# Kernel optimization log

Measured on AMD Instinct MI355X. Metric: run time of the kernel, lower is better.

Reference implementation:

```python
import jax, jax.numpy as jnp
import numpy as np

B, N, D, H = 128, 32768, 768, 16
DH = D // H          # per-head hidden_size = memory_dim // num_heads = 48
BETA = 0.25          # scaling (inverse temperature)
STEPS = 5            # update_steps_max
TOPK = 4


def _ln(x, g, b):
    # torch nn.LayerNorm over last dim (biased variance, eps=1e-5), affine
    m = jnp.mean(x, axis=-1, keepdims=True)
    v = jnp.var(x, axis=-1, keepdims=True)
    return (x - m) * jax.lax.rsqrt(v + 1e-5) * g + b


def _l2norm(x):
    # F.normalize(x, dim=-1): x / max(||x||, 1e-12)
    n = jnp.linalg.norm(x, axis=-1, keepdims=True)
    return x / jnp.maximum(n, 1e-12)


def setup_inputs() -> dict:
    key = jax.random.key(0)
    ks = jax.random.split(key, 8)
    s = 0.05  # weight init scale to keep activations sane
    return {
        "query_embedding": jax.random.normal(ks[0], (B, D), jnp.float32),
        "memory_bank": jax.random.normal(ks[1], (N, D), jnp.float32),
        "ln_k_g": jnp.ones((D,), jnp.float32), "ln_k_b": jnp.zeros((D,), jnp.float32),
        "ln_q_g": jnp.ones((D,), jnp.float32), "ln_q_b": jnp.zeros((D,), jnp.float32),
        "ln_v_g": jnp.ones((D,), jnp.float32), "ln_v_b": jnp.zeros((D,), jnp.float32),
        "Wq": jax.random.normal(ks[2], (D, D), jnp.float32) * s, "bq": jnp.zeros((D,), jnp.float32),
        "Wk": jax.random.normal(ks[3], (D, D), jnp.float32) * s, "bk": jnp.zeros((D,), jnp.float32),
        "Wv": jax.random.normal(ks[4], (D, D), jnp.float32) * s, "bv": jnp.zeros((D,), jnp.float32),
        "Wo": jax.random.normal(ks[5], (D, D), jnp.float32) * s, "bo": jnp.zeros((D,), jnp.float32),
        "W1": jax.random.normal(ks[6], (D, D), jnp.float32) * s, "b1": jnp.zeros((D,), jnp.float32),
        "W2": jax.random.normal(ks[7], (D, D), jnp.float32) * s, "b2": jnp.zeros((D,), jnp.float32),
    }


def reference(query_embedding, memory_bank, ln_k_g, ln_k_b, ln_q_g, ln_q_b,
              ln_v_g, ln_v_b, Wq, bq, Wk, bk, Wv, bv, Wo, bo, W1, b1, W2, b2):
    # Affine LayerNorms on stored pattern, state pattern, pattern projection.
    # memory_bank is shared across the batch, so normalize/project it ONCE
    # instead of materializing the (B, N, D) expand from the torch code.
    stored = _ln(memory_bank, ln_k_g, ln_k_b)        # (N, D)
    state = _ln(query_embedding, ln_q_g, ln_q_b)     # (B, D) -- state pattern, seq len 1
    projp = _ln(memory_bank, ln_v_g, ln_v_b)         # (N, D)

    k = (stored @ Wk.T + bk).reshape(N, H, DH)       # (N, H, dh)
    v = (projp @ Wv.T + bv).reshape(N, H, DH)        # (N, H, dh)
    q = (state @ Wq.T + bq).reshape(B, H, DH)        # (B, H, dh)

    # Hopfield convergence: xi <- softmax(beta * xi K^T) K, repeated STEPS times
    def step(xi, _):
        attn = jax.nn.softmax(BETA * jnp.einsum('bhd,nhd->bhn', xi, k), axis=-1)
        return jnp.einsum('bhn,nhd->bhd', attn, k), None

    xi, _ = jax.lax.scan(step, q, None, length=STEPS)

    # Final readout against the (separately normalized) pattern projection V
    attn = jax.nn.softmax(BETA * jnp.einsum('bhd,nhd->bhn', xi, k), axis=-1)  # (B, H, N)
    converged = jnp.einsum('bhn,nhd->bhd', attn, v).reshape(B, D) @ Wo.T + bo  # (B, D)

    # Retrieval head: residual + MLP + cosine-sim logits + top-k
    combined = query_embedding + converged
    rq = jax.nn.relu(combined @ W1.T + b1) @ W2.T + b2
    logits = (_l2norm(rq) @ _l2norm(memory_bank).T) * 20.0   # (B, N)
    top_indices = jax.lax.top_k(logits, TOPK)[1]              # (B, TOPK)
    return top_indices, logits
```

## Files before the change

kernel.cpp:

```cpp
#include <hip/hip_runtime.h>
#include <math.h>

#define NTOT 32768
#define DMODEL 768
#define BSZ 128
#define NHEAD 16
#define DH 48
#define BETA 0.25f

typedef _Float16 f16;
typedef f16 f16x8 __attribute__((ext_vector_type(8)));
typedef f16 f16x4 __attribute__((ext_vector_type(4)));
typedef float f32x4 __attribute__((ext_vector_type(4)));

__global__ __launch_bounds__(256)
void row_stats(const float* __restrict__ X, int M, float* __restrict__ mean,
               float* __restrict__ rstd, float* __restrict__ l2inv) {
  const int row = blockIdx.x * 4 + (threadIdx.x >> 6);
  const int lane = threadIdx.x & 63;
  if (row >= M) return;
  const float* x = X + (size_t)row * DMODEL;
  float s = 0.f, s2 = 0.f;
  for (int i = lane; i < DMODEL; i += 64) {
    float v = x[i];
    s += v; s2 += v * v;
  }
#pragma unroll
  for (int off = 32; off; off >>= 1) {
    s  += __shfl_xor(s, off);
    s2 += __shfl_xor(s2, off);
  }
  if (lane == 0) {
    float mu = s * (1.f / DMODEL);
    float var = s2 * (1.f / DMODEL) - mu * mu;
    mean[row] = mu;
    rstd[row] = rsqrtf(var + 1e-5f);
    if (l2inv) l2inv[row] = 1.f / fmaxf(sqrtf(s2), 1e-12f);
  }
}

__global__ __launch_bounds__(256)
void norm_split_mb(const float* __restrict__ mb, const float* __restrict__ mean,
                   const float* __restrict__ rstd, f16* __restrict__ nh_hi,
                   f16* __restrict__ nh_lo) {
  const int row = blockIdx.x * 4 + (threadIdx.x >> 6);
  const int lane = threadIdx.x & 63;
  const float mu = mean[row];
  const float rs = rstd[row];
  const float* x = mb + (size_t)row * DMODEL;
  f16* oh = nh_hi + (size_t)row * DMODEL;
  f16* ol = nh_lo + (size_t)row * DMODEL;
  for (int d = lane * 4; d < DMODEL; d += 256) {
    const float4 v = *(const float4*)(x + d);
    const float s[4] = {(v.x - mu) * rs, (v.y - mu) * rs,
                        (v.z - mu) * rs, (v.w - mu) * rs};
    f16x4 h4, l4;
#pragma unroll
    for (int j = 0; j < 4; j++) {
      const f16 h = (f16)s[j];
      h4[j] = h;
      l4[j] = (f16)(s[j] - (float)h);
    }
    *(f16x4*)(oh + d) = h4;
    *(f16x4*)(ol + d) = l4;
  }
}

__global__ __launch_bounds__(256)
void prep_w(const float* __restrict__ Wk, const float* __restrict__ bk,
            const float* __restrict__ gk, const float* __restrict__ blnk,
            const float* __restrict__ Wv, const float* __restrict__ bv,
            const float* __restrict__ gv, const float* __restrict__ blnv,
            f16* __restrict__ Wc_hi, f16* __restrict__ Wc_lo,
            float* __restrict__ biasc) {
  const int o = blockIdx.x * 4 + (threadIdx.x >> 6);
  const int lane = threadIdx.x & 63;
  const bool isK = o < DMODEL;
  const float* W = isK ? (Wk + (size_t)o * DMODEL)
                       : (Wv + (size_t)(o - DMODEL) * DMODEL);
  const float* g   = isK ? gk : gv;
  const float* bln = isK ? blnk : blnv;
  float bacc = 0.f;
  for (int d = lane * 4; d < DMODEL; d += 256) {
    const float4 wv = *(const float4*)(W + d);
    const float4 g4 = *(const float4*)(g + d);
    const float4 b4 = *(const float4*)(bln + d);
    bacc += wv.x * b4.x + wv.y * b4.y + wv.z * b4.z + wv.w * b4.w;
    const float sv[4] = {wv.x * g4.x * 16.f, wv.y * g4.y * 16.f,
                         wv.z * g4.z * 16.f, wv.w * g4.w * 16.f};
    f16x4 h4, l4;
#pragma unroll
    for (int j = 0; j < 4; j++) {
      const f16 h = (f16)sv[j];
      h4[j] = h;
      l4[j] = (f16)(sv[j] - (float)h);
    }
    *(f16x4*)(Wc_hi + (size_t)o * DMODEL + d) = h4;
    *(f16x4*)(Wc_lo + (size_t)o * DMODEL + d) = l4;
  }
#pragma unroll
  for (int off = 32; off; off >>= 1) bacc += __shfl_xor(bacc, off);
  if (lane == 0) biasc[o] = (isK ? bk[o] : bv[o - DMODEL]) + bacc;
}

__global__ __launch_bounds__(256)
void proj_dual_mfma(const f16* __restrict__ nh_hi, const f16* __restrict__ nh_lo,
                    const f16* __restrict__ Wc_hi, const f16* __restrict__ Wc_lo,
                    const float* __restrict__ biasc,
                    f16* __restrict__ k_hi, f16* __restrict__ k_lo,
                    f16* __restrict__ v_hi, f16* __restrict__ v_lo) {
  __shared__ __align__(16) f16 As[128][64];
  __shared__ __align__(16) f16 Bs[128][64];
  const int t = threadIdx.x;
  const int n0 = blockIdx.x * 128;
  const int m0 = blockIdx.y * 128;
  const int w = t >> 6, lane = t & 63;
  const int l15 = lane & 15, lq = lane >> 4;
  const int wm = w >> 1, wn = w & 1;
  const int sc = (lane & 7) ^ (lane >> 3);
  const int srow = lane >> 3;

  f32x4 acc[4][4];
#pragma unroll
  for (int a = 0; a < 4; a++)
#pragma unroll
    for (int b = 0; b < 4; b++)
#pragma unroll
      for (int r = 0; r < 4; r++) acc[a][b][r] = 0.f;

  for (int k0 = 0; k0 < DMODEL; k0 += 32) {
    __syncthreads();
#pragma unroll
    for (int i = 0; i < 4; i++) {
      const int rb = (w * 4 + i) * 8;
      const f16* asrc = ((sc < 4) ? nh_hi : nh_lo) +
          (size_t)(m0 + rb + srow) * DMODEL + k0 + (sc & 3) * 8;
      __builtin_amdgcn_global_load_lds(
          (__attribute__((address_space(1))) void*)asrc,
          (__attribute__((address_space(3))) void*)&As[rb][0], 16, 0, 0);
      const f16* bsrc = ((sc < 4) ? Wc_hi : Wc_lo) +
          (size_t)(n0 + rb + srow) * DMODEL + k0 + (sc & 3) * 8;
      __builtin_amdgcn_global_load_lds(
          (__attribute__((address_space(1))) void*)bsrc,
          (__attribute__((address_space(3))) void*)&Bs[rb][0], 16, 0, 0);
    }
    __syncthreads();

    f16x8 nhh[4], nhl[4];
#pragma unroll
    for (int fm = 0; fm < 4; fm++) {
      const int row = wm * 64 + fm * 16 + l15;
      const int e = row & 7;
      nhh[fm] = *(const f16x8*)&As[row][(lq ^ e) * 8];
      nhl[fm] = *(const f16x8*)&As[row][((lq + 4) ^ e) * 8];
    }
    f16x8 wh[4], wl[4];
#pragma unroll
    for (int fo = 0; fo < 4; fo++) {
      const int row = wn * 64 + fo * 16 + l15;
      const int e = row & 7;
      wh[fo] = *(const f16x8*)&Bs[row][(lq ^ e) * 8];
      wl[fo] = *(const f16x8*)&Bs[row][((lq + 4) ^ e) * 8];
    }
#pragma unroll
    for (int fo = 0; fo < 4; fo++)
#pragma unroll
      for (int fm = 0; fm < 4; fm++) {
        f32x4 a = acc[fo][fm];
        a = __builtin_amdgcn_mfma_f32_16x16x32_f16(wh[fo], nhh[fm], a, 0, 0, 0);
        a = __builtin_amdgcn_mfma_f32_16x16x32_f16(wh[fo], nhl[fm], a, 0, 0, 0);
        a = __builtin_amdgcn_mfma_f32_16x16x32_f16(wl[fo], nhh[fm], a, 0, 0, 0);
        acc[fo][fm] = a;
      }
  }
  const int oc = n0 + wn * 64;
  const bool isK = oc < DMODEL;
  f16* oh = isK ? k_hi : v_hi;
  f16* ol = isK ? k_lo : v_lo;
  const int obase = (isK ? oc : oc - DMODEL) + lq * 4;
#pragma unroll
  for (int fo = 0; fo < 4; fo++) {
    const float4 bb = *(const float4*)(biasc + oc + fo * 16 + lq * 4);
    const float bbv[4] = {bb.x, bb.y, bb.z, bb.w};
    const int o = obase + fo * 16;
#pragma unroll
    for (int fm = 0; fm < 4; fm++) {
      const size_t moff = (size_t)(m0 + wm * 64 + fm * 16 + l15) * DMODEL + o;
      f16x4 h4, l4;
#pragma unroll
      for (int r = 0; r < 4; r++) {
        const float v = acc[fo][fm][r] * 0.0625f + bbv[r];
        const f16 h = (f16)v;
        h4[r] = h;
        l4[r] = (f16)(v - (float)h);
      }
      *(f16x4*)(oh + moff) = h4;
      *(f16x4*)(ol + moff) = l4;
    }
  }
}

__global__ __launch_bounds__(256)
void ln_gemm_f32(const float* __restrict__ A, const float* __restrict__ mean,
                 const float* __restrict__ rstd, const float* __restrict__ g,
                 const float* __restrict__ bln, const float* __restrict__ W,
                 const float* __restrict__ bias, float* __restrict__ out) {
  __shared__ float As[16][68];
  __shared__ float Ws[16][68];
  const int t = threadIdx.x;
  const int m0 = blockIdx.y << 6, n0 = blockIdx.x << 6;
  const int tm = t >> 4, tn = t & 15;
  const int lr = t >> 2;
  const int lk = (t & 3) << 2;
  const float muL = mean[m0 + lr];
  const float rsL = rstd[m0 + lr];
  float acc[4][4] = {};
  for (int k0 = 0; k0 < DMODEL; k0 += 16) {
    float4 a4 = *(const float4*)(A + (size_t)(m0 + lr) * DMODEL + k0 + lk);
    float4 g4 = *(const float4*)(g + k0 + lk);
    float4 b4 = *(const float4*)(bln + k0 + lk);
    As[lk + 0][lr] = (a4.x - muL) * rsL * g4.x + b4.x;
    As[lk + 1][lr] = (a4.y - muL) * rsL * g4.y + b4.y;
    As[lk + 2][lr] = (a4.z - muL) * rsL * g4.z + b4.z;
    As[lk + 3][lr] = (a4.w - muL) * rsL * g4.w + b4.w;
    float4 w4 = *(const float4*)(W + (size_t)(n0 + lr) * DMODEL + k0 + lk);
    Ws[lk + 0][lr] = w4.x;
    Ws[lk + 1][lr] = w4.y;
    Ws[lk + 2][lr] = w4.z;
    Ws[lk + 3][lr] = w4.w;
    __syncthreads();
#pragma unroll
    for (int kk = 0; kk < 16; kk++) {
      const float4 av = *(const float4*)(&As[kk][tm * 4]);
      const float4 bv = *(const float4*)(&Ws[kk][tn * 4]);
      const float a[4] = {av.x, av.y, av.z, av.w};
      const float b[4] = {bv.x, bv.y, bv.z, bv.w};
#pragma unroll
      for (int i = 0; i < 4; i++)
#pragma unroll
        for (int j = 0; j < 4; j++) acc[i][j] += a[i] * b[j];
    }
    __syncthreads();
  }
  const float4 bia = *(const float4*)(bias + n0 + tn * 4);
  const float bb[4] = {bia.x, bia.y, bia.z, bia.w};
#pragma unroll
  for (int i = 0; i < 4; i++) {
    const int m = m0 + tm * 4 + i;
    float4 o4;
    o4.x = acc[i][0] + bb[0];
    o4.y = acc[i][1] + bb[1];
    o4.z = acc[i][2] + bb[2];
    o4.w = acc[i][3] + bb[3];
    *(float4*)(out + (size_t)m * DMODEL + n0 + tn * 4) = o4;
  }
}

__global__ __launch_bounds__(256)
void gemm_bias(const float* __restrict__ A, const float* __restrict__ W,
               const float* __restrict__ bias, const float* __restrict__ add,
               float* __restrict__ out, int relu) {
  __shared__ float As[16][68];
  __shared__ float Ws[16][68];
  const int t = threadIdx.x;
  const int m0 = blockIdx.y << 6, n0 = blockIdx.x << 6;
  const int tm = t >> 4, tn = t & 15;
  const int lr = t >> 2;
  const int lk = (t & 3) << 2;
  float acc[4][4] = {};
  for (int k0 = 0; k0 < DMODEL; k0 += 16) {
    float4 a4 = *(const float4*)(A + (size_t)(m0 + lr) * DMODEL + k0 + lk);
    As[lk + 0][lr] = a4.x;
    As[lk + 1][lr] = a4.y;
    As[lk + 2][lr] = a4.z;
    As[lk + 3][lr] = a4.w;
    float4 w4 = *(const float4*)(W + (size_t)(n0 + lr) * DMODEL + k0 + lk);
    Ws[lk + 0][lr] = w4.x;
    Ws[lk + 1][lr] = w4.y;
    Ws[lk + 2][lr] = w4.z;
    Ws[lk + 3][lr] = w4.w;
    __syncthreads();
#pragma unroll
    for (int kk = 0; kk < 16; kk++) {
      const float4 av = *(const float4*)(&As[kk][tm * 4]);
      const float4 bv = *(const float4*)(&Ws[kk][tn * 4]);
      const float a[4] = {av.x, av.y, av.z, av.w};
      const float b[4] = {bv.x, bv.y, bv.z, bv.w};
#pragma unroll
      for (int i = 0; i < 4; i++)
#pragma unroll
        for (int j = 0; j < 4; j++) acc[i][j] += a[i] * b[j];
    }
    __syncthreads();
  }
  const float4 bia = *(const float4*)(bias + n0 + tn * 4);
  const float bb[4] = {bia.x, bia.y, bia.z, bia.w};
#pragma unroll
  for (int i = 0; i < 4; i++) {
    const int m = m0 + tm * 4 + i;
    float v[4];
#pragma unroll
    for (int j = 0; j < 4; j++) v[j] = acc[i][j] + bb[j];
    if (add) {
      const float4 a4 = *(const float4*)(add + (size_t)m * DMODEL + n0 + tn * 4);
      v[0] += a4.x; v[1] += a4.y; v[2] += a4.z; v[3] += a4.w;
    }
    if (relu) {
#pragma unroll
      for (int j = 0; j < 4; j++) v[j] = fmaxf(v[j], 0.f);
    }
    float4 o4 = {v[0], v[1], v[2], v[3]};
    *(float4*)(out + (size_t)m * DMODEL + n0 + tn * 4) = o4;
  }
}

__global__ __launch_bounds__(256)
void logits_gemm(const float* __restrict__ A, const float* __restrict__ Bm,
                 const float* __restrict__ ainv, const float* __restrict__ binv,
                 float* __restrict__ out) {
  __shared__ float As[16][68];
  __shared__ float Ws[16][68];
  const int t = threadIdx.x;
  const int m0 = blockIdx.y << 6, n0 = blockIdx.x << 6;
  const int tm = t >> 4, tn = t & 15;
  const int lr = t >> 2;
  const int lk = (t & 3) << 2;
  float acc[4][4] = {};
  for (int k0 = 0; k0 < DMODEL; k0 += 16) {
    float4 a4 = *(const float4*)(A + (size_t)(m0 + lr) * DMODEL + k0 + lk);
    As[lk + 0][lr] = a4.x;
    As[lk + 1][lr] = a4.y;
    As[lk + 2][lr] = a4.z;
    As[lk + 3][lr] = a4.w;
    float4 w4 = *(const float4*)(Bm + (size_t)(n0 + lr) * DMODEL + k0 + lk);
    Ws[lk + 0][lr] = w4.x;
    Ws[lk + 1][lr] = w4.y;
    Ws[lk + 2][lr] = w4.z;
    Ws[lk + 3][lr] = w4.w;
    __syncthreads();
#pragma unroll
    for (int kk = 0; kk < 16; kk++) {
      const float4 av = *(const float4*)(&As[kk][tm * 4]);
      const float4 bv = *(const float4*)(&Ws[kk][tn * 4]);
      const float a[4] = {av.x, av.y, av.z, av.w};
      const float b[4] = {bv.x, bv.y, bv.z, bv.w};
#pragma unroll
      for (int i = 0; i < 4; i++)
#pragma unroll
        for (int j = 0; j < 4; j++) acc[i][j] += a[i] * b[j];
    }
    __syncthreads();
  }
  const float4 bi4 = *(const float4*)(binv + n0 + tn * 4);
  const float bi[4] = {bi4.x, bi4.y, bi4.z, bi4.w};
#pragma unroll
  for (int i = 0; i < 4; i++) {
    const int m = m0 + tm * 4 + i;
    const float sa = 20.f * ainv[m];
    float4 o4;
    o4.x = acc[i][0] * sa * bi[0];
    o4.y = acc[i][1] * sa * bi[1];
    o4.z = acc[i][2] * sa * bi[2];
    o4.w = acc[i][3] * sa * bi[3];
    *(float4*)(out + (size_t)m * NTOT + n0 + tn * 4) = o4;
  }
}

__global__ __launch_bounds__(256)
void split_xi_k(const float* __restrict__ xi, f16* __restrict__ hi,
                f16* __restrict__ lo) {
  const int i = blockIdx.x * 256 + threadIdx.x;
  float4 v = ((const float4*)xi)[i];
  float s[4] = {v.x * BETA, v.y * BETA, v.z * BETA, v.w * BETA};
  f16x4 h4, l4;
#pragma unroll
  for (int j = 0; j < 4; j++) {
    f16 h = (f16)s[j];
    h4[j] = h;
    l4[j] = (f16)(s[j] - (float)h);
  }
  ((f16x4*)hi)[i] = h4;
  ((f16x4*)lo)[i] = l4;
}

#define FCHUNK 64
#define FROWS (NTOT / FCHUNK)

__global__ __launch_bounds__(256)
void flash_round(const f16* __restrict__ k_hi, const f16* __restrict__ k_lo,
                 const f16* __restrict__ val_hi, const f16* __restrict__ val_lo,
                 const f16* __restrict__ xi_hi, const f16* __restrict__ xi_lo,
                 float* __restrict__ part_ml, float* __restrict__ part_o) {
  const int h = blockIdx.y, chunk = blockIdx.x;
  const int tid = threadIdx.x, w = tid >> 6, lane = tid & 63;
  const int l15 = lane & 15, lq = lane >> 4;
  const int b0 = w * 32;

  __shared__ __align__(16) f16 krow[2][32][56];
  __shared__ __align__(16) f16 vT[2][48][40];
  __shared__ __align__(16) f16 pHi[4][32][40];
  __shared__ __align__(16) f16 pLo[4][32][40];

  const f16x8 zf = {};
  f16x8 xqh[2][2], xql[2][2];
#pragma unroll
  for (int bt = 0; bt < 2; bt++) {
    const size_t xoff = (size_t)(b0 + bt * 16 + l15) * DMODEL + h * DH;
    xqh[bt][0] = *(const f16x8*)(xi_hi + xoff + lq * 8);
    xql[bt][0] = *(const f16x8*)(xi_lo + xoff + lq * 8);
    const size_t xo1 = xoff + 32 + (lq & 1) * 8;
    f16x8 th = *(const f16x8*)(xi_hi + xo1);
    f16x8 tl = *(const f16x8*)(xi_lo + xo1);
    xqh[bt][1] = (lq < 2) ? th : zf;
    xql[bt][1] = (lq < 2) ? tl : zf;
  }

  float m[2] = {-1e30f, -1e30f}, lsum[2] = {0.f, 0.f};
  f32x4 O[3][2];
#pragma unroll
  for (int mt = 0; mt < 3; mt++)
#pragma unroll
    for (int bt = 0; bt < 2; bt++)
#pragma unroll
      for (int j = 0; j < 4; j++) O[mt][bt][j] = 0.f;

  const int nbase = chunk * FROWS;
  for (int it = 0; it < FROWS / 32; it++) {
    const int gn0 = nbase + it * 32;
    __syncthreads();
    for (int j = tid; j < 384; j += 256) {
      const int tsel = j / 192;
      const int q = j - tsel * 192;
      const int r = q / 6;
      const int d0 = (q - r * 6) * 8;
      const size_t goff = (size_t)(gn0 + r) * DMODEL + h * DH + d0;
      const f16* kp = (tsel ? k_lo : k_hi) + goff;
      const f16* vp = (tsel ? val_lo : val_hi) + goff;
      f16x8 kv = *(const f16x8*)kp;
      f16x8 vv = *(const f16x8*)vp;
      *(f16x8*)&krow[tsel][r][d0] = kv;
#pragma unroll
      for (int jj = 0; jj < 8; jj++) vT[tsel][d0 + jj][r] = vv[jj];
    }
    __syncthreads();

    f16x8 akh[2][2], akl[2][2];
#pragma unroll
    for (int nt = 0; nt < 2; nt++) {
      const int row = nt * 16 + l15;
      akh[nt][0] = *(const f16x8*)&krow[0][row][lq * 8];
      akl[nt][0] = *(const f16x8*)&krow[1][row][lq * 8];
      f16x8 t0 = *(const f16x8*)&krow[0][row][32 + (lq & 1) * 8];
      f16x8 t1 = *(const f16x8*)&krow[1][row][32 + (lq & 1) * 8];
      akh[nt][1] = (lq < 2) ? t0 : zf;
      akl[nt][1] = (lq < 2) ? t1 : zf;
    }
    f32x4 S[2][2];
#pragma unroll
    for (int nt = 0; nt < 2; nt++)
#pragma unroll
      for (int bt = 0; bt < 2; bt++) {
        f32x4 s = {};
        s = __builtin_amdgcn_mfma_f32_16x16x32_f16(akh[nt][0], xqh[bt][0], s, 0, 0, 0);
        s = __builtin_amdgcn_mfma_f32_16x16x32_f16(akh[nt][1], xqh[bt][1], s, 0, 0, 0);
        s = __builtin_amdgcn_mfma_f32_16x16x32_f16(akh[nt][0], xql[bt][0], s, 0, 0, 0);
        s = __builtin_amdgcn_mfma_f32_16x16x32_f16(akh[nt][1], xql[bt][1], s, 0, 0, 0);
        s = __builtin_amdgcn_mfma_f32_16x16x32_f16(akl[nt][0], xqh[bt][0], s, 0, 0, 0);
        s = __builtin_amdgcn_mfma_f32_16x16x32_f16(akl[nt][1], xqh[bt][1], s, 0, 0, 0);
        S[nt][bt] = s;
      }
    float sc[2];
#pragma unroll
    for (int bt = 0; bt < 2; bt++) {
      float mx = S[0][bt][0];
#pragma unroll
      for (int r = 1; r < 4; r++) mx = fmaxf(mx, S[0][bt][r]);
#pragma unroll
      for (int r = 0; r < 4; r++) mx = fmaxf(mx, S[1][bt][r]);
      mx = fmaxf(mx, __shfl_xor(mx, 16));
      mx = fmaxf(mx, __shfl_xor(mx, 32));
      const float mnew = fmaxf(m[bt], mx);
      sc[bt] = __expf(m[bt] - mnew);
      float ps = 0.f;
#pragma unroll
      for (int nt = 0; nt < 2; nt++) {
        f16x4 ph, pl;
#pragma unroll
        for (int r = 0; r < 4; r++) {
          const float p = __expf(S[nt][bt][r] - mnew);
          ps += p;
          const f16 hh = (f16)p;
          ph[r] = hh;
          pl[r] = (f16)(p - (float)hh);
        }
        *(f16x4*)&pHi[w][bt * 16 + l15][nt * 16 + lq * 4] = ph;
        *(f16x4*)&pLo[w][bt * 16 + l15][nt * 16 + lq * 4] = pl;
      }
      ps += __shfl_xor(ps, 16);
      ps += __shfl_xor(ps, 32);
      lsum[bt] = lsum[bt] * sc[bt] + ps;
      m[bt] = mnew;
    }
    __asm__ volatile("s_waitcnt lgkmcnt(0)" ::: "memory");
    f16x8 avh[3], avl[3];
#pragma unroll
    for (int mt = 0; mt < 3; mt++) {
      avh[mt] = *(const f16x8*)&vT[0][mt * 16 + l15][lq * 8];
      avl[mt] = *(const f16x8*)&vT[1][mt * 16 + l15][lq * 8];
    }
    f16x8 pbh[2], pbl[2];
#pragma unroll
    for (int bt = 0; bt < 2; bt++) {
      pbh[bt] = *(const f16x8*)&pHi[w][bt * 16 + l15][lq * 8];
      pbl[bt] = *(const f16x8*)&pLo[w][bt * 16 + l15][lq * 8];
    }
#pragma unroll
    for (int mt = 0; mt < 3; mt++)
#pragma unroll
      for (int bt = 0; bt < 2; bt++) {
#pragma unroll
        for (int j = 0; j < 4; j++) O[mt][bt][j] *= sc[bt];
        f32x4 o = O[mt][bt];
        o = __builtin_amdgcn_mfma_f32_16x16x32_f16(avh[mt], pbh[bt], o, 0, 0, 0);
        o = __builtin_amdgcn_mfma_f32_16x16x32_f16(avh[mt], pbl[bt], o, 0, 0, 0);
        o = __builtin_amdgcn_mfma_f32_16x16x32_f16(avl[mt], pbh[bt], o, 0, 0, 0);
        O[mt][bt] = o;
      }
  }
  const int pc = h * FCHUNK + chunk;
  if (lq == 0) {
#pragma unroll
    for (int bt = 0; bt < 2; bt++) {
      float* pm = part_ml + ((size_t)pc * BSZ + b0 + bt * 16 + l15) * 2;
      pm[0] = m[bt];
      pm[1] = lsum[bt];
    }
  }
#pragma unroll
  for (int mt = 0; mt < 3; mt++)
#pragma unroll
    for (int bt = 0; bt < 2; bt++) {
      float* po = part_o + ((size_t)pc * BSZ + b0 + bt * 16 + l15) * 48 +
                  mt * 16 + lq * 4;
      *(f32x4*)po = O[mt][bt];
    }
}

__global__ __launch_bounds__(64)
void hopfield_combine(const float* __restrict__ part_ml,
                      const float* __restrict__ part_o, float* __restrict__ dst) {
  const int bh = blockIdx.x;
  const int h = bh >> 7, b = bh & 127;
  const int c = threadIdx.x;
  __shared__ float w[64];
  const float* pm = part_ml + ((size_t)(h * 64 + c) * BSZ + b) * 2;
  const float mp = pm[0];
  const float lp = pm[1];
  float M = mp;
#pragma unroll
  for (int off = 32; off; off >>= 1) M = fmaxf(M, __shfl_xor(M, off));
  const float wp = __expf(mp - M);
  w[c] = wp;
  float L = lp * wp;
#pragma unroll
  for (int off = 32; off; off >>= 1) L += __shfl_xor(L, off);
  __syncthreads();
  if (c < DH) {
    float o = 0.f;
    for (int p = 0; p < 64; p++)
      o += part_o[((size_t)(h * 64 + p) * BSZ + b) * 48 + c] * w[p];
    dst[(size_t)b * DMODEL + h * DH + c] = o / L;
  }
}

__global__ __launch_bounds__(256)
void topk_kernel(const float* __restrict__ logits, float* __restrict__ outIdx) {
  const int b = blockIdx.x;
  const int t = threadIdx.x;
  const float* row = logits + (size_t)b * NTOT;
  float v[4] = {-1e30f, -1e30f, -1e30f, -1e30f};
  int id[4] = {0x7fffffff, 0x7fffffff, 0x7fffffff, 0x7fffffff};
  for (int n = t; n < NTOT; n += 256) {
    const float x = row[n];
    if (x > v[3]) {
      v[3] = x; id[3] = n;
#pragma unroll
      for (int s = 3; s > 0; s--) {
        const bool sw = (v[s] > v[s - 1]) || (v[s] == v[s - 1] && id[s] < id[s - 1]);
        if (sw) {
          float tv = v[s]; v[s] = v[s - 1]; v[s - 1] = tv;
          int ti = id[s]; id[s] = id[s - 1]; id[s - 1] = ti;
        }
      }
    }
  }
  __shared__ float sv[256][4];
  __shared__ int si[256][4];
#pragma unroll
  for (int j = 0; j < 4; j++) { sv[t][j] = v[j]; si[t][j] = id[j]; }
  for (int str = 128; str >= 1; str >>= 1) {
    __syncthreads();
    if (t < str) {
      float a[4], c[4];
      int ai[4], ci[4];
#pragma unroll
      for (int j = 0; j < 4; j++) {
        a[j] = sv[t][j]; ai[j] = si[t][j];
        c[j] = sv[t + str][j]; ci[j] = si[t + str][j];
      }
      float rv[4]; int ri[4];
      int p = 0, q = 0;
#pragma unroll
      for (int oo = 0; oo < 4; oo++) {
        const bool ta = (a[p] > c[q]) || (a[p] == c[q] && ai[p] < ci[q]);
        if (ta) { rv[oo] = a[p]; ri[oo] = ai[p]; p++; }
        else    { rv[oo] = c[q]; ri[oo] = ci[q]; q++; }
      }
#pragma unroll
      for (int j = 0; j < 4; j++) { sv[t][j] = rv[j]; si[t][j] = ri[j]; }
    }
  }
  if (t == 0) {
#pragma unroll
    for (int j = 0; j < 4; j++) outIdx[b * 4 + j] = (float)si[0][j];
  }
}

extern "C" void kernel_launch(void* const* d_in, const int* in_sizes, int n_in,
                              void* d_out, int out_size, void* d_ws, size_t ws_size,
                              hipStream_t stream) {
  const float* qe    = (const float*)d_in[0];
  const float* mb    = (const float*)d_in[1];
  const float* ln_kg = (const float*)d_in[2];
  const float* ln_kb = (const float*)d_in[3];
  const float* ln_qg = (const float*)d_in[4];
  const float* ln_qb = (const float*)d_in[5];
  const float* ln_vg = (const float*)d_in[6];
  const float* ln_vb = (const float*)d_in[7];
  const float* Wq = (const float*)d_in[8];
  const float* bq = (const float*)d_in[9];
  const float* Wk = (const float*)d_in[10];
  const float* bk = (const float*)d_in[11];
  const float* Wv = (const float*)d_in[12];
  const float* bv = (const float*)d_in[13];
  const float* Wo = (const float*)d_in[14];
  const float* bo = (const float*)d_in[15];
  const float* W1 = (const float*)d_in[16];
  const float* b1 = (const float*)d_in[17];
  const float* W2 = (const float*)d_in[18];
  const float* b2 = (const float*)d_in[19];

  float* out = (float*)d_out;
  float* logits = out + BSZ * 4;

  float* ws = (float*)d_ws;
  size_t off = 0;
  auto alloc = [&](size_t n) { float* p = ws + off; off += n; return p; };
  const size_t ND2 = (size_t)NTOT * DMODEL / 2;
  float* mb_mean = alloc(NTOT);
  float* mb_rstd = alloc(NTOT);
  float* mb_l2i  = alloc(NTOT);
  float* q_mean  = alloc(128);
  float* q_rstd  = alloc(128);
  float* rq_inv  = alloc(128);
  float* pad_    = alloc(384);
  f16* k_hi = (f16*)alloc(ND2);
  f16* k_lo = (f16*)alloc(ND2);
  f16* v_hi = (f16*)alloc(ND2);
  f16* v_lo = (f16*)alloc(ND2);
  f16* nh_hi = (f16*)alloc(ND2);
  f16* nh_lo = (f16*)alloc(ND2);
  float* part_ml = alloc((size_t)NHEAD * FCHUNK * BSZ * 2);
  float* part_o  = alloc((size_t)NHEAD * FCHUNK * BSZ * 48);
  float* xi   = alloc((size_t)BSZ * DMODEL);
  float* conv = alloc((size_t)BSZ * DMODEL);
  float* comb = alloc((size_t)BSZ * DMODEL);
  float* h1   = alloc((size_t)BSZ * DMODEL);
  f16* xi_hi = (f16*)alloc((size_t)BSZ * DMODEL / 2);
  f16* xi_lo = (f16*)alloc((size_t)BSZ * DMODEL / 2);
  f16* Wc_hi = (f16*)alloc((size_t)2 * DMODEL * DMODEL / 2);
  f16* Wc_lo = (f16*)alloc((size_t)2 * DMODEL * DMODEL / 2);
  float* biasc = alloc(2 * DMODEL);
  (void)ws_size; (void)in_sizes; (void)n_in; (void)out_size; (void)pad_;

  row_stats<<<NTOT / 4, 256, 0, stream>>>(mb, NTOT, mb_mean, mb_rstd, mb_l2i);
  row_stats<<<BSZ / 4, 256, 0, stream>>>(qe, BSZ, q_mean, q_rstd, nullptr);
  norm_split_mb<<<NTOT / 4, 256, 0, stream>>>(mb, mb_mean, mb_rstd, nh_hi, nh_lo);
  prep_w<<<2 * DMODEL / 4, 256, 0, stream>>>(Wk, bk, ln_kg, ln_kb,
                                             Wv, bv, ln_vg, ln_vb,
                                             Wc_hi, Wc_lo, biasc);

  proj_dual_mfma<<<dim3(2 * DMODEL / 128, NTOT / 128), 256, 0, stream>>>(
      nh_hi, nh_lo, Wc_hi, Wc_lo, biasc, k_hi, k_lo, v_hi, v_lo);
  ln_gemm_f32<<<dim3(DMODEL / 64, BSZ / 64), 256, 0, stream>>>(
      qe, q_mean, q_rstd, ln_qg, ln_qb, Wq, bq, xi);

  for (int r = 0; r < 6; r++) {
    const f16* valHi = (r == 5) ? v_hi : k_hi;
    const f16* valLo = (r == 5) ? v_lo : k_lo;
    float* dst = (r == 5) ? conv : xi;
    split_xi_k<<<96, 256, 0, stream>>>(xi, xi_hi, xi_lo);
    flash_round<<<dim3(FCHUNK, NHEAD), 256, 0, stream>>>(
        k_hi, k_lo, valHi, valLo, xi_hi, xi_lo, part_ml, part_o);
    hopfield_combine<<<BSZ * NHEAD, 64, 0, stream>>>(part_ml, part_o, dst);
  }

  gemm_bias<<<dim3(DMODEL / 64, BSZ / 64), 256, 0, stream>>>(conv, Wo, bo, qe, comb, 0);
  gemm_bias<<<dim3(DMODEL / 64, BSZ / 64), 256, 0, stream>>>(comb, W1, b1, nullptr, h1, 1);
  float* rq = conv;
  gemm_bias<<<dim3(DMODEL / 64, BSZ / 64), 256, 0, stream>>>(h1, W2, b2, nullptr, rq, 0);

  row_stats<<<BSZ / 4, 256, 0, stream>>>(rq, BSZ, q_mean, q_rstd, rq_inv);
  logits_gemm<<<dim3(NTOT / 64, BSZ / 64), 256, 0, stream>>>(rq, mb, rq_inv, mb_l2i, logits);

  topk_kernel<<<BSZ, 256, 0, stream>>>(logits, out);
}
```

Measured before the change: 1.489 ms.

## Compute cosine logits with split-fp16 MFMA on layer-normed bank, fuse mb stats

Replaces the fp32 SIMT logits GEMM with a split-precision (hi/lo fp16) MFMA GEMM. It reuses the already-normalised memory bank halves and recovers raw-bank dot products algebraically as x = n*std + mu, with per-row constants c1 and c2. It also fuses the memory-bank row statistics into the normalise-and-split kernel, removing one full pass over the 100MB bank. The algebraic reconstruction risks precision loss from cancellation between the std and mean terms, which could change top-k ordering.

```diff
diff --git a/kernel.cpp b/kernel.cpp
--- a/kernel.cpp
+++ b/kernel.cpp
@@ -40,29 +40,87 @@
 }
 
 __global__ __launch_bounds__(256)
-void norm_split_mb(const float* __restrict__ mb, const float* __restrict__ mean,
-                   const float* __restrict__ rstd, f16* __restrict__ nh_hi,
-                   f16* __restrict__ nh_lo) {
+void stats_norm_mb(const float* __restrict__ mb, f16* __restrict__ nh_hi,
+                   f16* __restrict__ nh_lo, float* __restrict__ c1,
+                   float* __restrict__ c2) {
   const int row = blockIdx.x * 4 + (threadIdx.x >> 6);
   const int lane = threadIdx.x & 63;
-  const float mu = mean[row];
-  const float rs = rstd[row];
   const float* x = mb + (size_t)row * DMODEL;
+  float v[12];
+  float s = 0.f, s2 = 0.f;
+#pragma unroll
+  for (int j = 0; j < 3; j++) {
+    const float4 v4 = *(const float4*)(x + lane * 4 + j * 256);
+    v[j * 4 + 0] = v4.x; v[j * 4 + 1] = v4.y;
+    v[j * 4 + 2] = v4.z; v[j * 4 + 3] = v4.w;
+    s += v4.x + v4.y + v4.z + v4.w;
+    s2 += v4.x * v4.x + v4.y * v4.y + v4.z * v4.z + v4.w * v4.w;
+  }
+#pragma unroll
+  for (int off = 32; off; off >>= 1) {
+    s  += __shfl_xor(s, off);
+    s2 += __shfl_xor(s2, off);
+  }
+  const float mu = s * (1.f / DMODEL);
+  const float var = s2 * (1.f / DMODEL) - mu * mu;
+  const float istd = sqrtf(var + 1e-5f);
+  const float rs = 1.f / istd;
   f16* oh = nh_hi + (size_t)row * DMODEL;
   f16* ol = nh_lo + (size_t)row * DMODEL;
-  for (int d = lane * 4; d < DMODEL; d += 256) {
-    const float4 v = *(const float4*)(x + d);
-    const float s[4] = {(v.x - mu) * rs, (v.y - mu) * rs,
-                        (v.z - mu) * rs, (v.w - mu) * rs};
+#pragma unroll
+  for (int j = 0; j < 3; j++) {
     f16x4 h4, l4;
 #pragma unroll
-    for (int j = 0; j < 4; j++) {
-      const f16 h = (f16)s[j];
-      h4[j] = h;
-      l4[j] = (f16)(s[j] - (float)h);
+    for (int q = 0; q < 4; q++) {
+      const float sv = (v[j * 4 + q] - mu) * rs;
+      const f16 h = (f16)sv;
+      h4[q] = h;
+      l4[q] = (f16)(sv - (float)h);
+    }
+    *(f16x4*)(oh + lane * 4 + j * 256) = h4;
+    *(f16x4*)(ol + lane * 4 + j * 256) = l4;
+  }
+  if (lane == 0) {
+    const float l2i = 1.f / fmaxf(sqrtf(s2), 1e-12f);
+    c1[row] = 20.f * l2i * istd;
+    c2[row] = 20.f * l2i * mu;
+  }
+}
+
+__global__ __launch_bounds__(256)
+void rq_prep(const float* __restrict__ rq, f16* __restrict__ hi,
+             f16* __restrict__ lo, float* __restrict__ ainv,
+             float* __restrict__ rqsum) {
+  const int row = blockIdx.x * 4 + (threadIdx.x >> 6);
+  const int lane = threadIdx.x & 63;
+  const float* x = rq + (size_t)row * DMODEL;
+  f16* oh = hi + (size_t)row * DMODEL;
+  f16* ol = lo + (size_t)row * DMODEL;
+  float s = 0.f, s2 = 0.f;
+#pragma unroll
+  for (int j = 0; j < 3; j++) {
+    const int d = lane * 4 + j * 256;
+    const float4 v4 = *(const float4*)(x + d);
+    const float vv[4] = {v4.x, v4.y, v4.z, v4.w};
+    f16x4 h4, l4;
+#pragma unroll
+    for (int q = 0; q < 4; q++) {
+      s += vv[q]; s2 += vv[q] * vv[q];
+      const f16 h = (f16)vv[q];
+      h4[q] = h;
+      l4[q] = (f16)(vv[q] - (float)h);
     }
     *(f16x4*)(oh + d) = h4;
     *(f16x4*)(ol + d) = l4;
+  }
+#pragma unroll
+  for (int off = 32; off; off >>= 1) {
+    s  += __shfl_xor(s, off);
+    s2 += __shfl_xor(s2, off);
+  }
+  if (lane == 0) {
+    rqsum[row] = s;
+    ainv[row] = 1.f / fmaxf(sqrtf(s2), 1e-12f);
   }
 }
 
@@ -196,6 +254,98 @@
       }
       *(f16x4*)(oh + moff) = h4;
       *(f16x4*)(ol + moff) = l4;
+    }
+  }
+}
+
+__global__ __launch_bounds__(256)
+void logits_mfma(const f16* __restrict__ nh_hi, const f16* __restrict__ nh_lo,
+                 const f16* __restrict__ rq_hi, const f16* __restrict__ rq_lo,
+                 const float* __restrict__ c1, const float* __restrict__ c2,
+                 const float* __restrict__ ainv, const float* __restrict__ rqsum,
+                 float* __restrict__ out) {
+  __shared__ __align__(16) f16 As[128][64];
+  __shared__ __align__(16) f16 Bs[128][64];
+  const int t = threadIdx.x;
+  const int n0 = blockIdx.x * 128;
+  const int w = t >> 6, lane = t & 63;
+  const int l15 = lane & 15, lq = lane >> 4;
+  const int wm = w >> 1, wn = w & 1;
+  const int sc = (lane & 7) ^ (lane >> 3);
+  const int srow = lane >> 3;
+
+  f32x4 acc[4][4];
+#pragma unroll
+  for (int a = 0; a < 4; a++)
+#pragma unroll
+    for (int b = 0; b < 4; b++)
+#pragma unroll
+      for (int r = 0; r < 4; r++) acc[a][b][r] = 0.f;
+
+  for (int k0 = 0; k0 < DMODEL; k0 += 32) {
+    __syncthreads();
+#pragma unroll
+    for (int i = 0; i < 4; i++) {
+      const int rb = (w * 4 + i) * 8;
+      const f16* asrc = ((sc < 4) ? nh_hi : nh_lo) +
+          (size_t)(n0 + rb + srow) * DMODEL + k0 + (sc & 3) * 8;
+      __builtin_amdgcn_global_load_lds(
+          (__attribute__((address_space(1))) void*)asrc,
+          (__attribute__((address_space(3))) void*)&As[rb][0], 16, 0, 0);
+      const f16* bsrc = ((sc < 4) ? rq_hi : rq_lo) +
+          (size_t)(rb + srow) * DMODEL + k0 + (sc & 3) * 8;
+      __builtin_amdgcn_global_load_lds(
+          (__attribute__((address_space(1))) void*)bsrc,
+          (__attribute__((address_space(3))) void*)&Bs[rb][0], 16, 0, 0);
+    }
+    __syncthreads();
+
+    f16x8 ah[4], al[4];
+#pragma unroll
+    for (int fo = 0; fo < 4; fo++) {
+      const int row = wn * 64 + fo * 16 + l15;
+      const int e = row & 7;
+      ah[fo] = *(const f16x8*)&As[row][(lq ^ e) * 8];
+      al[fo] = *(const f16x8*)&As[row][((lq + 4) ^ e) * 8];
+    }
+    f16x8 bh[4], bl[4];
+#pragma unroll
+    for (int fm = 0; fm < 4; fm++) {
+      const int row = wm * 64 + fm * 16 + l15;
+      const int e = row & 7;
+      bh[fm] = *(const f16x8*)&Bs[row][(lq ^ e) * 8];
+      bl[fm] = *(const f16x8*)&Bs[row][((lq + 4) ^ e) * 8];
+    }
+#pragma unroll
+    for (int fo = 0; fo < 4; fo++)
+#pragma unroll
+      for (int fm = 0; fm < 4; fm++) {
+        f32x4 a = acc[fo][fm];
+        a = __builtin_amdgcn_mfma_f32_16x16x32_f16(ah[fo], bh[fm], a, 0, 0, 0);
+        a = __builtin_amdgcn_mfma_f32_16x16x32_f16(ah[fo], bl[fm], a, 0, 0, 0);
+        a = __builtin_amdgcn_mfma_f32_16x16x32_f16(al[fo], bh[fm], a, 0, 0, 0);
+        acc[fo][fm] = a;
+      }
+  }
+#pragma unroll
+  for (int fm = 0; fm < 4; fm++) {
+    const int b = wm * 64 + fm * 16 + l15;
+    const float am = ainv[b];
+    const float rs = rqsum[b];
+#pragma unroll
+    for (int fo = 0; fo < 4; fo++) {
+      const int nb = n0 + wn * 64 + fo * 16 + lq * 4;
+      const float4 c1v = *(const float4*)(c1 + nb);
+      const float4 c2v = *(const float4*)(c2 + nb);
+      const float c1a[4] = {c1v.x, c1v.y, c1v.z, c1v.w};
+      const float c2a[4] = {c2v.x, c2v.y, c2v.z, c2v.w};
+      float4 o4;
+      float ov[4];
+#pragma unroll
+      for (int r = 0; r < 4; r++)
+        ov[r] = am * (acc[fo][fm][r] * c1a[r] + rs * c2a[r]);
+      o4.x = ov[0]; o4.y = ov[1]; o4.z = ov[2]; o4.w = ov[3];
+      *(float4*)(out + (size_t)b * NTOT + nb) = o4;
     }
   }
 }
@@ -315,58 +465,6 @@
 }
 
 __global__ __launch_bounds__(256)
-void logits_gemm(const float* __restrict__ A, const float* __restrict__ Bm,
-                 const float* __restrict__ ainv, const float* __restrict__ binv,
-                 float* __restrict__ out) {
-  __shared__ float As[16][68];
-  __shared__ float Ws[16][68];
-  const int t = threadIdx.x;
-  const int m0 = blockIdx.y << 6, n0 = blockIdx.x << 6;
-  const int tm = t >> 4, tn = t & 15;
-  const int lr = t >> 2;
-  const int lk = (t & 3) << 2;
-  float acc[4][4] = {};
-  for (int k0 = 0; k0 < DMODEL; k0 += 16) {
-    float4 a4 = *(const float4*)(A + (size_t)(m0 + lr) * DMODEL + k0 + lk);
-    As[lk + 0][lr] = a4.x;
-    As[lk + 1][lr] = a4.y;
-    As[lk + 2][lr] = a4.z;
-    As[lk + 3][lr] = a4.w;
-    float4 w4 = *(const float4*)(Bm + (size_t)(n0 + lr) * DMODEL + k0 + lk);
-    Ws[lk + 0][lr] = w4.x;
-    Ws[lk + 1][lr] = w4.y;
-    Ws[lk + 2][lr] = w4.z;
-    Ws[lk + 3][lr] = w4.w;
-    __syncthreads();
-#pragma unroll
-    for (int kk = 0; kk < 16; kk++) {
-      const float4 av = *(const float4*)(&As[kk][tm * 4]);
-      const float4 bv = *(const float4*)(&Ws[kk][tn * 4]);
-      const float a[4] = {av.x, av.y, av.z, av.w};
-      const float b[4] = {bv.x, bv.y, bv.z, bv.w};
-#pragma unroll
-      for (int i = 0; i < 4; i++)
-#pragma unroll
-        for (int j = 0; j < 4; j++) acc[i][j] += a[i] * b[j];
-    }
-    __syncthreads();
-  }
-  const float4 bi4 = *(const float4*)(binv + n0 + tn * 4);
-  const float bi[4] = {bi4.x, bi4.y, bi4.z, bi4.w};
-#pragma unroll
-  for (int i = 0; i < 4; i++) {
-    const int m = m0 + tm * 4 + i;
-    const float sa = 20.f * ainv[m];
-    float4 o4;
-    o4.x = acc[i][0] * sa * bi[0];
-    o4.y = acc[i][1] * sa * bi[1];
-    o4.z = acc[i][2] * sa * bi[2];
-    o4.w = acc[i][3] * sa * bi[3];
-    *(float4*)(out + (size_t)m * NTOT + n0 + tn * 4) = o4;
-  }
-}
-
-__global__ __launch_bounds__(256)
 void split_xi_k(const float* __restrict__ xi, f16* __restrict__ hi,
                 f16* __restrict__ lo) {
   const int i = blockIdx.x * 256 + threadIdx.x;
@@ -657,13 +755,13 @@
   size_t off = 0;
   auto alloc = [&](size_t n) { float* p = ws + off; off += n; return p; };
   const size_t ND2 = (size_t)NTOT * DMODEL / 2;
-  float* mb_mean = alloc(NTOT);
-  float* mb_rstd = alloc(NTOT);
-  float* mb_l2i  = alloc(NTOT);
+  float* c1      = alloc(NTOT);
+  float* c2      = alloc(NTOT);
   float* q_mean  = alloc(128);
   float* q_rstd  = alloc(128);
   float* rq_inv  = alloc(128);
-  float* pad_    = alloc(384);
+  float* rq_sum  = alloc(128);
+  float* pad_    = alloc(256);
   f16* k_hi = (f16*)alloc(ND2);
   f16* k_lo = (f16*)alloc(ND2);
   f16* v_hi = (f16*)alloc(ND2);
@@ -678,14 +776,15 @@
   float* h1   = alloc((size_t)BSZ * DMODEL);
   f16* xi_hi = (f16*)alloc((size_t)BSZ * DMODEL / 2);
   f16* xi_lo = (f16*)alloc((size_t)BSZ * DMODEL / 2);
+  f16* rq_hi = (f16*)alloc((size_t)BSZ * DMODEL / 2);
+  f16* rq_lo = (f16*)alloc((size_t)BSZ * DMODEL / 2);
   f16* Wc_hi = (f16*)alloc((size_t)2 * DMODEL * DMODEL / 2);
   f16* Wc_lo = (f16*)alloc((size_t)2 * DMODEL * DMODEL / 2);
   float* biasc = alloc(2 * DMODEL);
   (void)ws_size; (void)in_sizes; (void)n_in; (void)out_size; (void)pad_;
 
-  row_stats<<<NTOT / 4, 256, 0, stream>>>(mb, NTOT, mb_mean, mb_rstd, mb_l2i);
   row_stats<<<BSZ / 4, 256, 0, stream>>>(qe, BSZ, q_mean, q_rstd, nullptr);
-  norm_split_mb<<<NTOT / 4, 256, 0, stream>>>(mb, mb_mean, mb_rstd, nh_hi, nh_lo);
+  stats_norm_mb<<<NTOT / 4, 256, 0, stream>>>(mb, nh_hi, nh_lo, c1, c2);
   prep_w<<<2 * DMODEL / 4, 256, 0, stream>>>(Wk, bk, ln_kg, ln_kb,
                                              Wv, bv, ln_vg, ln_vb,
                                              Wc_hi, Wc_lo, biasc);
@@ -710,8 +809,9 @@
   float* rq = conv;
   gemm_bias<<<dim3(DMODEL / 64, BSZ / 64), 256, 0, stream>>>(h1, W2, b2, nullptr, rq, 0);
 
-  row_stats<<<BSZ / 4, 256, 0, stream>>>(rq, BSZ, q_mean, q_rstd, rq_inv);
-  logits_gemm<<<dim3(NTOT / 64, BSZ / 64), 256, 0, stream>>>(rq, mb, rq_inv, mb_l2i, logits);
+  rq_prep<<<BSZ / 4, 256, 0, stream>>>(rq, rq_hi, rq_lo, rq_inv, rq_sum);
+  logits_mfma<<<NTOT / 128, 256, 0, stream>>>(nh_hi, nh_lo, rq_hi, rq_lo,
+                                              c1, c2, rq_inv, rq_sum, logits);
 
   topk_kernel<<<BSZ, 256, 0, stream>>>(logits, out);
 }
```

New measurement: 1.374 ms. -7.7%, faster.
